# Performance work log

Measured on AMD Instinct MI355X. Metric: run time of the kernel, lower is better.

## Reference

```python
import jax, jax.numpy as jnp
import numpy as np

SWISH_BETA = 0.8
ALPHA = 0.2

def swish(x):
    return x * jax.nn.sigmoid(SWISH_BETA * x)

def setup_inputs() -> dict:
    key = jax.random.key(0)
    ks = jax.random.split(key, 8)
    B, t_in, T, n_nodes, n_in, n_heads, kp1 = 4, 12, 24, 20000, 16, 8, 9
    x = jax.random.normal(ks[0], (B, t_in, n_nodes, n_in), dtype=jnp.float32)
    nearest_nodes = jax.random.randint(ks[1], (n_nodes, kp1), 0, n_nodes + 1)
    agg_w = jax.random.normal(ks[2], (1, kp1), dtype=jnp.float32) / np.sqrt(kp1)
    agg_b = jax.random.normal(ks[3], (1,), dtype=jnp.float32) * 0.01
    mh_w = jax.random.normal(ks[4], (n_heads, 1), dtype=jnp.float32)
    mh_b = jax.random.normal(ks[5], (n_heads,), dtype=jnp.float32) * 0.01
    shrink_w = jax.random.normal(ks[6], (T - t_in, t_in * n_heads), dtype=jnp.float32) / np.sqrt(t_in * n_heads)
    shrink_b = jax.random.normal(ks[7], (T - t_in,), dtype=jnp.float32) * 0.01
    return {"x": x, "nearest_nodes": nearest_nodes, "agg_w": agg_w, "agg_b": agg_b,
            "mh_w": mh_w, "mh_b": mh_b, "shrink_w": shrink_w, "shrink_b": shrink_b}

def reference(x, nearest_nodes, agg_w, agg_b, mh_w, mh_b, shrink_w, shrink_b):
    B, t_in, n_nodes, n_in = x.shape
    n_heads = mh_w.shape[0]
    # pad node axis with a zero row (pad index == n_nodes)
    pad_x = jnp.concatenate([x, jnp.zeros_like(x[:, :, :1])], axis=2)  # (B,t,n+1,c)
    # gather k+1 neighbors per node
    x_nn = pad_x[:, :, nearest_nodes]  # (B,t,n,k+1,c)
    # agg_fc: Linear(k+1 -> 1) over neighbor axis
    x_agg = jnp.einsum('btnkc,k->btnc', x_nn, agg_w[0]) + agg_b[0]  # (B,t,n,c)
    # multihead_fc: swish then Linear(1 -> n_heads)
    x_agg = swish(x_agg)
    x_agg = x_agg[..., None] * mh_w[:, 0] + mh_b  # (B,t,n,c,H)
    x_agg = jnp.swapaxes(x_agg, -1, -2)  # (B,t,n,H,c)
    # temporal alpha blend (vectorized, uses pre-blend values)
    x_agg = jnp.concatenate(
        [x_agg[:, :1], (1.0 - ALPHA) * x_agg[:, 1:] + ALPHA * x_agg[:, :-1]], axis=1)
    # (B,t,n,H,c) -> (B,n,c,t,H) -> (B,n,c,t*H)
    agg = jnp.transpose(x_agg, (0, 2, 4, 1, 3)).reshape(B, n_nodes, n_in, t_in * n_heads)
    y = jax.nn.selu(agg @ shrink_w.T + shrink_b)  # (B,n,c,T-t_in)
    y = jnp.transpose(y, (0, 3, 1, 2))  # (B,T-t_in,n,c)
    return jnp.concatenate([x, y], axis=1)  # (B,T,n,c)
```

## Files before the change

kernel.cpp:

```cpp
#include <hip/hip_runtime.h>

#define BB 4
#define T_IN 12
#define T_OUT 24
#define NNODE 20000
#define CC 16
#define KP1 9
#define NH 8
#define JJ 12
#define NODES_PER_BLK 64
#define CHUNKS_PER_SLICE 313
#define NXCD 8
#define NSLICE (BB * T_IN)
#define SLICES_PER_XCD (NSLICE / NXCD)

__device__ __forceinline__ float swish1(float s) {
    return s / (1.f + __expf(-0.8f * s));
}

__global__ __launch_bounds__(256) void gather_swish(
    const float4* __restrict__ x,
    const int* __restrict__ nn,
    const float* __restrict__ agg_w,
    const float* __restrict__ agg_b,
    float4* __restrict__ out)
{
    const int xcd = blockIdx.x & (NXCD - 1);
    const int j = blockIdx.x >> 3;
    const int slice_local = j / CHUNKS_PER_SLICE;
    const int chunk = j - slice_local * CHUNKS_PER_SLICE;
    const int slice = xcd * SLICES_PER_XCD + slice_local;
    const int b = slice / T_IN;
    const int t = slice - b * T_IN;

    const int tid = threadIdx.x;
    const int r = tid >> 2;
    const int q = tid & 3;
    const int n = chunk * NODES_PER_BLK + r;
    if (n >= NNODE) return;

    int idx[KP1];
    float w[KP1];
#pragma unroll
    for (int k = 0; k < KP1; ++k) {
        idx[k] = nn[n * KP1 + k];
        w[k] = agg_w[k];
        if (idx[k] >= NNODE) { idx[k] = 0; w[k] = 0.f; }
    }

    const float4* xs = x + (size_t)slice * (NNODE * 4) + q;
    const float bias = agg_b[0];
    float4 s; s.x = bias; s.y = bias; s.z = bias; s.w = bias;
#pragma unroll
    for (int k = 0; k < KP1; ++k) {
        float4 v = xs[(size_t)idx[k] * 4];
        s.x += w[k] * v.x; s.y += w[k] * v.y;
        s.z += w[k] * v.z; s.w += w[k] * v.w;
    }
    s.x = swish1(s.x); s.y = swish1(s.y); s.z = swish1(s.z); s.w = swish1(s.w);

    float4 xv = xs[(size_t)n * 4];
    const size_t out_b = (size_t)b * (T_OUT * NNODE * 4);
    out[out_b + (size_t)t * (NNODE * 4) + n * 4 + q] = xv;
    out[out_b + (size_t)(T_IN + t) * (NNODE * 4) + n * 4 + q] = s;
}

__global__ __launch_bounds__(256) void ema_shrink(
    const float* __restrict__ mh_w,
    const float* __restrict__ mh_b,
    const float* __restrict__ shrink_w,
    const float* __restrict__ shrink_b,
    float4* __restrict__ out)
{
    __shared__ float sWc[JJ][T_IN];
    __shared__ float sBc[JJ];
    const int tid = threadIdx.x;

    if (tid < JJ * T_IN) {
        int jo = tid / T_IN, t = tid - jo * T_IN;
        float s = 0.f;
#pragma unroll
        for (int h = 0; h < NH; ++h)
            s += mh_w[h] * shrink_w[jo * (T_IN * NH) + t * NH + h];
        sWc[jo][t] = s;
    }
    if (tid < JJ) {
        float s = shrink_b[tid];
#pragma unroll
        for (int qq = 0; qq < T_IN * NH; ++qq)
            s += mh_b[qq & (NH - 1)] * shrink_w[tid * (T_IN * NH) + qq];
        sBc[tid] = s;
    }
    __syncthreads();

    const int g = blockIdx.x * 256 + tid;
    const int b = g / (NNODE * 4);
    const int rem = g - b * (NNODE * 4);
    const size_t base = ((size_t)b * T_OUT + T_IN) * (NNODE * 4) + rem;

    float4 a[T_IN];
#pragma unroll
    for (int t = 0; t < T_IN; ++t) a[t] = out[base + (size_t)t * (NNODE * 4)];

#pragma unroll
    for (int t = T_IN - 1; t >= 1; --t) {
        a[t].x = 0.8f * a[t].x + 0.2f * a[t - 1].x;
        a[t].y = 0.8f * a[t].y + 0.2f * a[t - 1].y;
        a[t].z = 0.8f * a[t].z + 0.2f * a[t - 1].z;
        a[t].w = 0.8f * a[t].w + 0.2f * a[t - 1].w;
    }

#pragma unroll
    for (int jo = 0; jo < JJ; ++jo) {
        float4 s;
        s.x = sBc[jo]; s.y = sBc[jo]; s.z = sBc[jo]; s.w = sBc[jo];
#pragma unroll
        for (int t = 0; t < T_IN; ++t) {
            float wv = sWc[jo][t];
            s.x += a[t].x * wv; s.y += a[t].y * wv;
            s.z += a[t].z * wv; s.w += a[t].w * wv;
        }
        s.x = (s.x > 0.f) ? 1.0507009873554805f * s.x
                          : 1.7580993408473766f * (__expf(s.x) - 1.f);
        s.y = (s.y > 0.f) ? 1.0507009873554805f * s.y
                          : 1.7580993408473766f * (__expf(s.y) - 1.f);
        s.z = (s.z > 0.f) ? 1.0507009873554805f * s.z
                          : 1.7580993408473766f * (__expf(s.z) - 1.f);
        s.w = (s.w > 0.f) ? 1.0507009873554805f * s.w
                          : 1.7580993408473766f * (__expf(s.w) - 1.f);
        out[base + (size_t)jo * (NNODE * 4)] = s;
    }
}

extern "C" void kernel_launch(void* const* d_in, const int* in_sizes, int n_in,
                              void* d_out, int out_size, void* d_ws, size_t ws_size,
                              hipStream_t stream) {
    const float* x        = (const float*)d_in[0];
    const int*   nn       = (const int*)d_in[1];
    const float* agg_w    = (const float*)d_in[2];
    const float* agg_b    = (const float*)d_in[3];
    const float* mh_w     = (const float*)d_in[4];
    const float* mh_b     = (const float*)d_in[5];
    const float* shrink_w = (const float*)d_in[6];
    const float* shrink_b = (const float*)d_in[7];
    float4* out = (float4*)d_out;

    gather_swish<<<NXCD * SLICES_PER_XCD * CHUNKS_PER_SLICE, 256, 0, stream>>>(
        (const float4*)x, nn, agg_w, agg_b, out);
    ema_shrink<<<(BB * NNODE * 4) / 256, 256, 0, stream>>>(
        mh_w, mh_b, shrink_w, shrink_b, out);
}
```

Baseline: 75.60 us.

## Process two time slices per block, stage neighbor indices in LDS, use nontemporal stores

After: 77.48 us. +2.5%, slower.

```diff
diff --git a/kernel.cpp b/kernel.cpp
--- a/kernel.cpp
+++ b/kernel.cpp
@@ -13,9 +13,19 @@
 #define NXCD 8
 #define NSLICE (BB * T_IN)
 #define SLICES_PER_XCD (NSLICE / NXCD)
+#define PAIRS_PER_XCD (SLICES_PER_XCD / 2)
+
+typedef __attribute__((ext_vector_type(4))) float f4;
 
 __device__ __forceinline__ float swish1(float s) {
     return s / (1.f + __expf(-0.8f * s));
+}
+__device__ __forceinline__ void nt_store4(const float4& v, float4* p) {
+    __builtin_nontemporal_store(*(const f4*)&v, (f4*)p);
+}
+__device__ __forceinline__ float4 nt_load4(const float4* p) {
+    f4 v = __builtin_nontemporal_load((const f4*)p);
+    return *(float4*)&v;
 }
 
 __global__ __launch_bounds__(256) void gather_swish(
@@ -25,44 +35,65 @@
     const float* __restrict__ agg_b,
     float4* __restrict__ out)
 {
+    __shared__ int sNN[NODES_PER_BLK * KP1];
+
     const int xcd = blockIdx.x & (NXCD - 1);
     const int j = blockIdx.x >> 3;
-    const int slice_local = j / CHUNKS_PER_SLICE;
-    const int chunk = j - slice_local * CHUNKS_PER_SLICE;
-    const int slice = xcd * SLICES_PER_XCD + slice_local;
-    const int b = slice / T_IN;
-    const int t = slice - b * T_IN;
+    const int pair = j / CHUNKS_PER_SLICE;
+    const int chunk = j - pair * CHUNKS_PER_SLICE;
+    const int slice0 = xcd * SLICES_PER_XCD + pair * 2;
+    const int b = slice0 / T_IN;
+    const int t0 = slice0 - b * T_IN;
 
     const int tid = threadIdx.x;
+    const int n_base = chunk * NODES_PER_BLK;
+
+    for (int i = tid; i < NODES_PER_BLK * KP1; i += 256) {
+        int gi = n_base * KP1 + i;
+        sNN[i] = (gi < NNODE * KP1) ? nn[gi] : NNODE;
+    }
+    __syncthreads();
+
     const int r = tid >> 2;
     const int q = tid & 3;
-    const int n = chunk * NODES_PER_BLK + r;
+    const int n = n_base + r;
     if (n >= NNODE) return;
 
     int idx[KP1];
     float w[KP1];
 #pragma unroll
     for (int k = 0; k < KP1; ++k) {
-        idx[k] = nn[n * KP1 + k];
+        idx[k] = sNN[r * KP1 + k];
         w[k] = agg_w[k];
         if (idx[k] >= NNODE) { idx[k] = 0; w[k] = 0.f; }
     }
 
-    const float4* xs = x + (size_t)slice * (NNODE * 4) + q;
     const float bias = agg_b[0];
-    float4 s; s.x = bias; s.y = bias; s.z = bias; s.w = bias;
+    const float4* xs0 = x + (size_t)slice0 * (NNODE * 4) + q;
+    const float4* xs1 = xs0 + (NNODE * 4);
+
+    float4 s0, s1;
+    s0.x = s0.y = s0.z = s0.w = bias;
+    s1.x = s1.y = s1.z = s1.w = bias;
 #pragma unroll
     for (int k = 0; k < KP1; ++k) {
-        float4 v = xs[(size_t)idx[k] * 4];
-        s.x += w[k] * v.x; s.y += w[k] * v.y;
-        s.z += w[k] * v.z; s.w += w[k] * v.w;
+        float4 v0 = xs0[(size_t)idx[k] * 4];
+        float4 v1 = xs1[(size_t)idx[k] * 4];
+        float wk = w[k];
+        s0.x += wk * v0.x; s0.y += wk * v0.y; s0.z += wk * v0.z; s0.w += wk * v0.w;
+        s1.x += wk * v1.x; s1.y += wk * v1.y; s1.z += wk * v1.z; s1.w += wk * v1.w;
     }
-    s.x = swish1(s.x); s.y = swish1(s.y); s.z = swish1(s.z); s.w = swish1(s.w);
+    s0.x = swish1(s0.x); s0.y = swish1(s0.y); s0.z = swish1(s0.z); s0.w = swish1(s0.w);
+    s1.x = swish1(s1.x); s1.y = swish1(s1.y); s1.z = swish1(s1.z); s1.w = swish1(s1.w);
 
-    float4 xv = xs[(size_t)n * 4];
     const size_t out_b = (size_t)b * (T_OUT * NNODE * 4);
-    out[out_b + (size_t)t * (NNODE * 4) + n * 4 + q] = xv;
-    out[out_b + (size_t)(T_IN + t) * (NNODE * 4) + n * 4 + q] = s;
+    const size_t row = (size_t)n * 4 + q;
+    float4 xv0 = xs0[(size_t)n * 4];
+    float4 xv1 = xs1[(size_t)n * 4];
+    nt_store4(xv0, &out[out_b + (size_t)t0 * (NNODE * 4) + row]);
+    nt_store4(xv1, &out[out_b + (size_t)(t0 + 1) * (NNODE * 4) + row]);
+    nt_store4(s0, &out[out_b + (size_t)(T_IN + t0) * (NNODE * 4) + row]);
+    nt_store4(s1, &out[out_b + (size_t)(T_IN + t0 + 1) * (NNODE * 4) + row]);
 }
 
 __global__ __launch_bounds__(256) void ema_shrink(
@@ -100,7 +131,7 @@
 
     float4 a[T_IN];
 #pragma unroll
-    for (int t = 0; t < T_IN; ++t) a[t] = out[base + (size_t)t * (NNODE * 4)];
+    for (int t = 0; t < T_IN; ++t) a[t] = nt_load4(&out[base + (size_t)t * (NNODE * 4)]);
 
 #pragma unroll
     for (int t = T_IN - 1; t >= 1; --t) {
@@ -128,7 +159,7 @@
                           : 1.7580993408473766f * (__expf(s.z) - 1.f);
         s.w = (s.w > 0.f) ? 1.0507009873554805f * s.w
                           : 1.7580993408473766f * (__expf(s.w) - 1.f);
-        out[base + (size_t)jo * (NNODE * 4)] = s;
+        nt_store4(s, &out[base + (size_t)jo * (NNODE * 4)]);
     }
 }
 
@@ -145,7 +176,7 @@
     const float* shrink_b = (const float*)d_in[7];
     float4* out = (float4*)d_out;
 
-    gather_swish<<<NXCD * SLICES_PER_XCD * CHUNKS_PER_SLICE, 256, 0, stream>>>(
+    gather_swish<<<NXCD * PAIRS_PER_XCD * CHUNKS_PER_SLICE, 256, 0, stream>>>(
         (const float4*)x, nn, agg_w, agg_b, out);
     ema_shrink<<<(BB * NNODE * 4) / 256, 256, 0, stream>>>(
         mh_w, mh_b, shrink_w, shrink_b, out);
```
